# Kernel optimization log

Hardware: AMD Instinct MI355X
Metric: run time of the kernel (lower is better)

The kernel has to match this reference:

```python
import jax, jax.numpy as jnp
import numpy as np

KSIZE = 7
NSPIX = 196


def _unfold(x, k):
    # x: (T, C, H, W) -> (T, C, k*k, H, W), reflect padding, torch Unfold ordering
    p = (k - 1) // 2
    T, C, H, W = x.shape
    xp = jnp.pad(x, ((0, 0), (0, 0), (p, p), (p, p)), mode='reflect')
    return jnp.stack([xp[:, :, i:i + H, j:j + W] for i in range(k) for j in range(k)], axis=2)


def setup_inputs() -> dict:
    key = jax.random.key(0)
    k1, k2, k3, k4, k5 = jax.random.split(key, 5)
    T, C, H, W = 2, 64, 160, 160
    fan_in = C * KSIZE * KSIZE
    x = jax.random.normal(k1, (T, C, H, W), jnp.float32)
    spix = jax.random.randint(k2, (T, H, W), 0, NSPIX, jnp.int32)
    W_lin = jax.random.normal(k3, (C, fan_in), jnp.float32) / np.sqrt(fan_in)
    b_lin = jax.random.normal(k4, (C,), jnp.float32) * 0.01
    w_scale = jax.random.normal(k5, (C,), jnp.float32) / np.sqrt(C)
    b_scale = jnp.zeros((1,), jnp.float32)
    return {"x": x, "spix": spix, "W_lin": W_lin, "b_lin": b_lin,
            "w_scale": w_scale, "b_scale": b_scale}


def reference(x, spix, W_lin, b_lin, w_scale, b_scale):
    T, C, H, W = x.shape
    K2 = KSIZE * KSIZE
    O = W_lin.shape[0]
    p = (KSIZE - 1) // 2

    # unfold(x) with reflect padding -> patches (T, C, K2, H, W)
    patches = _unfold(x, KSIZE)

    # unfold(spix) -> neighbor superpixel ids per pixel (T, K2, H, W)
    sp = jnp.pad(spix, ((0, 0), (p, p), (p, p)), mode='reflect')
    nb = jnp.stack([sp[:, i:i + H, j:j + W] for i in range(KSIZE) for j in range(KSIZE)], axis=1)

    # per-frame superpixel mean pooling (bist.get_pooled_video): down (T, S, C)
    seg = (spix.astype(jnp.int32) + jnp.arange(T, dtype=jnp.int32)[:, None, None] * NSPIX).reshape(-1)
    feats = x.transpose(0, 2, 3, 1).reshape(-1, C)  # (T*H*W, C)
    sums = jax.ops.segment_sum(feats, seg, num_segments=T * NSPIX).reshape(T, NSPIX, C)
    cnts = jax.ops.segment_sum(jnp.ones((seg.shape[0],), x.dtype), seg,
                               num_segments=T * NSPIX).reshape(T, NSPIX, 1)
    down = sums / jnp.maximum(cnts, 1.0)

    # squared pairwise distances between superpixel means: pwd (T, S, S)
    sq = jnp.sum(down * down, axis=-1)
    pwd = jnp.maximum(sq[:, :, None] + sq[:, None, :]
                      - 2.0 * jnp.einsum('tsc,tuc->tsu', down, down), 0.0)

    # sims[t,k,h,w] = ||mean(spix[t,h,w]) - mean(nb[t,k,h,w])||^2
    tidx = jnp.arange(T)[:, None, None, None]
    sims = pwd[tidx, spix[:, None, :, :], nb]  # (T, K2, H, W)

    # scale = 10 * softplus(1x1-conv(x / ||x||_c))  -> (T, H, W)
    xn = x / (jnp.linalg.norm(x, axis=1, keepdims=True) + 1e-10)
    scale = 10.0 * jax.nn.softplus(jnp.einsum('c,tchw->thw', w_scale, xn) + b_scale[0])

    # apply_norm 'exp_max' over the kernel-tap axis
    rw = jnp.exp(-scale[:, None, :, :] * sims)  # (T, K2, H, W)
    rw = rw / (1e-5 + jnp.max(rw, axis=1, keepdims=True))

    # dynamic conv: out[t,o,h,w] = sum_{c,k} W[o,c,k] * patches[t,c,k,h,w] * rw[t,k,h,w] + b[o]
    out = jnp.einsum('ock,tckhw,tkhw->tohw', W_lin.reshape(O, C, K2), patches, rw)
    return out + b_lin[None, :, None, None]
```

## Files before the change

### kernel.cpp

```cpp
#include <hip/hip_runtime.h>
#include <math.h>

#define TT 2
#define CC 64
#define HH 160
#define WW 160
#define KS 7
#define K2 49
#define NSPIX 196
#define HWSZ (HH*WW)
#define PAD 3
#define OO 64
#define FANIN (CC*K2)
#define TS 8
#define PS (TS+KS-1)
#define NPOS (PS*PS)
#define XROW 72

#define NCHUNK 50
#define CHUNKPIX 512
#define NCG 8

typedef short short8 __attribute__((ext_vector_type(8)));
typedef float f32x16 __attribute__((ext_vector_type(16)));

__device__ __forceinline__ int reflect(int i, int n) {
    if (i < 0) i = -i;
    if (i >= n) i = 2*n - 2 - i;
    return i;
}

__device__ __forceinline__ unsigned short f2bf(float f) {
    unsigned int u = __float_as_uint(f);
    unsigned int r = (u + 0x7FFFu + ((u >> 16) & 1u)) >> 16;
    return (unsigned short)r;
}
__device__ __forceinline__ float bf2f(unsigned short s) {
    return __uint_as_float(((unsigned int)s) << 16);
}

__global__ void k_wb(const float* __restrict__ Wl, unsigned short* __restrict__ Wb) {
    int idx = blockIdx.x*256 + threadIdx.x;
    if (idx >= 2*K2*4*64*8) return;
    int j   = idx & 7;
    int ln  = (idx >> 3) & 63;
    int kc  = (idx >> 9) & 3;
    int tap = (idx >> 11) % K2;
    int qo  = idx / (K2 << 11);
    int o = qo*32 + (ln & 31);
    int c = kc*16 + (ln >> 5)*8 + j;
    Wb[idx] = f2bf(Wl[o*FANIN + c*K2 + tap]);
}

__global__ __launch_bounds__(256) void k_seg(const float* __restrict__ x,
                                             const int* __restrict__ spix,
                                             float* __restrict__ partials,
                                             float* __restrict__ cntp) {
    __shared__ float ls[8*200];
    __shared__ float lcnt[200];
    int tid = threadIdx.x;
    int cg = blockIdx.x & 7;
    int rest = blockIdx.x >> 3;
    int ch = rest % NCHUNK;
    int t  = rest / NCHUNK;

    for (int i = tid; i < 8*200; i += 256) ls[i] = 0.f;
    if (cg == 0) for (int i = tid; i < 200; i += 256) lcnt[i] = 0.f;
    __syncthreads();

    int base = ch*CHUNKPIX;
    const float* xb = x + ((size_t)t*CC + cg*8)*HWSZ;
    #pragma unroll
    for (int i = 0; i < CHUNKPIX; i += 256) {
        int pix = base + i + tid;
        int s = spix[t*HWSZ + pix];
        if (cg == 0) atomicAdd(&lcnt[s], 1.0f);
        #pragma unroll
        for (int j = 0; j < 8; ++j) atomicAdd(&ls[j*200 + s], xb[(size_t)j*HWSZ + pix]);
    }
    __syncthreads();

    float* pb = partials + ((size_t)(t*NCHUNK + ch)*NSPIX)*CC + cg*8;
    for (int i = tid; i < 8*NSPIX; i += 256) {
        int s = i >> 3, j = i & 7;
        pb[s*CC + j] = ls[j*200 + s];
    }
    if (cg == 0)
        for (int i = tid; i < NSPIX; i += 256)
            cntp[(t*NCHUNK + ch)*NSPIX + i] = lcnt[i];
}

__global__ __launch_bounds__(256) void k_red(const float* __restrict__ partials,
                                             const float* __restrict__ cntp,
                                             float* __restrict__ down,
                                             float* __restrict__ sq) {
    int ts = blockIdx.x*4 + threadIdx.y;
    if (ts >= TT*NSPIX) return;
    int t = ts / NSPIX, s = ts - t*NSPIX;
    int c = threadIdx.x;

    const float* pb = partials + ((size_t)t*NCHUNK*NSPIX + s)*CC + c;
    float acc = 0.f;
    #pragma unroll 10
    for (int ch = 0; ch < NCHUNK; ++ch) acc += pb[(size_t)ch*NSPIX*CC];

    float cv = (c < NCHUNK) ? cntp[(t*NCHUNK + c)*NSPIX + s] : 0.f;
    #pragma unroll
    for (int off = 1; off < 64; off <<= 1) cv += __shfl_xor(cv, off, 64);

    float d = acc / fmaxf(cv, 1.0f);
    down[ts*CC + c] = d;
    float v = d*d;
    #pragma unroll
    for (int off = 1; off < 64; off <<= 1) v += __shfl_xor(v, off, 64);
    if (c == 0) sq[ts] = v;
}

__global__ void k_pwd(const float* __restrict__ down, const float* __restrict__ sq,
                      float* __restrict__ pwd) {
    int tid = blockIdx.x*256 + threadIdx.x;
    if (tid >= TT*NSPIX*NSPIX) return;
    int t = tid / (NSPIX*NSPIX); int r = tid - t*NSPIX*NSPIX;
    int s = r / NSPIX, u = r - (r / NSPIX)*NSPIX;
    const float* ds = down + (t*NSPIX + s)*CC;
    const float* du = down + (t*NSPIX + u)*CC;
    float dot = 0.f;
    #pragma unroll 4
    for (int c = 0; c < CC; ++c) dot += ds[c]*du[c];
    float v = sq[t*NSPIX + s] + sq[t*NSPIX + u] - 2.f*dot;
    pwd[tid] = fmaxf(v, 0.f);
}

__global__ void k_scale(const float* __restrict__ x, const float* __restrict__ wsc,
                        const float* __restrict__ bsc, float* __restrict__ scale) {
    int pix = blockIdx.x*256 + threadIdx.x;
    if (pix >= TT*HWSZ) return;
    int t = pix / HWSZ, hw = pix - t*HWSZ;
    const float* xs = x + (size_t)t*CC*HWSZ + hw;
    float s1 = 0.f, s2 = 0.f;
    #pragma unroll 8
    for (int c = 0; c < CC; ++c) { float v = xs[c*HWSZ]; s1 += wsc[c]*v; s2 += v*v; }
    float z = s1/(sqrtf(s2) + 1e-10f) + bsc[0];
    float sp_ = (z > 0.f) ? z + log1pf(expf(-z)) : log1pf(expf(z));
    scale[pix] = 10.f*sp_;
}

__global__ __launch_bounds__(256, 4) void k_main(
    const float* __restrict__ x, const int* __restrict__ spix,
    const unsigned short* __restrict__ Wb, const float* __restrict__ b_lin,
    const float* __restrict__ pwd, const float* __restrict__ scale,
    float* __restrict__ out)
{
    __shared__ unsigned short xpT[NPOS*XROW];
    __shared__ unsigned short rwb[K2*64];
    __shared__ int   sp[NPOS];
    __shared__ float mxp[4*64];
    __shared__ float mxl[64];

    int bid = blockIdx.x;
    int t = bid / 400;
    int r = bid - t*400;
    int th0 = (r / 20)*TS, tw0 = (r - (r/20)*20)*TS;
    int tid = threadIdx.y*64 + threadIdx.x;

    for (int i = tid; i < NPOS; i += 256) {
        int rr = reflect(th0 + i/PS - PAD, HH);
        int cc = reflect(tw0 + i%PS - PAD, WW);
        sp[i] = spix[t*HWSZ + rr*WW + cc];
    }
    for (int i = tid; i < NPOS*32; i += 256) {
        int pos = i % NPOS;
        int cp  = i / NPOS;
        int rr = reflect(th0 + pos/PS - PAD, HH);
        int cc = reflect(tw0 + pos%PS - PAD, WW);
        const float* xs = x + ((size_t)t*CC + 2*cp)*HWSZ + rr*WW + cc;
        float v0 = xs[0];
        float v1 = xs[HWSZ];
        unsigned int pk = (unsigned int)f2bf(v0) | ((unsigned int)f2bf(v1) << 16);
        *(unsigned int*)&xpT[pos*XROW + cp*2] = pk;
    }
    __syncthreads();

    int p_ = threadIdx.x;
    int ty = threadIdx.y;
    int py0 = p_ >> 3, px0 = p_ & 7;
    {
        float sc = scale[t*HWSZ + (th0 + py0)*WW + (tw0 + px0)];
        int s0 = sp[(py0 + PAD)*PS + (px0 + PAD)];
        const float* pr = pwd + (t*NSPIX + s0)*NSPIX;
        float pmax = 0.f;
        for (int k = ty; k < K2; k += 4) {
            int di = k/KS, dj = k - di*KS;
            int nb = sp[(py0 + di)*PS + (px0 + dj)];
            float v = expf(-sc * pr[nb]);
            rwb[k*64 + p_] = f2bf(v);
            pmax = fmaxf(pmax, v);
        }
        mxp[ty*64 + p_] = pmax;
    }
    __syncthreads();
    if (ty == 0) {
        float m = fmaxf(fmaxf(mxp[p_], mxp[64 + p_]), fmaxf(mxp[128 + p_], mxp[192 + p_]));
        mxl[p_] = 1.f/(1e-5f + m);
    }
    __syncthreads();
    {
        float s = mxl[p_];
        for (int k = ty; k < K2; k += 4)
            rwb[k*64 + p_] = f2bf(bf2f(rwb[k*64 + p_]) * s);
    }
    __syncthreads();

    int ln = threadIdx.x;
    int wv = __builtin_amdgcn_readfirstlane(threadIdx.y);
    int qo = wv >> 1, qp = wv & 1;
    int p  = qp*32 + (ln & 31);
    int ppy = p >> 3, ppx = p & 7;
    int k8 = (ln >> 5)*8;

    const unsigned short* Wq = Wb + (size_t)qo*K2*4*512 + ln*8;

    f32x16 acc;
    #pragma unroll
    for (int i = 0; i < 16; ++i) acc[i] = 0.f;

    int di = 0, dj = 0;
    for (int tap = 0; tap < K2; ++tap) {
        const unsigned short* wt = Wq + tap*2048;
        short8 A0 = *(const short8*)(wt);
        short8 A1 = *(const short8*)(wt + 512);
        short8 A2 = *(const short8*)(wt + 1024);
        short8 A3 = *(const short8*)(wt + 1536);

        int pos = (ppy + di)*PS + (ppx + dj);
        const unsigned short* bb = &xpT[pos*XROW + k8];
        short8 B0 = *(const short8*)(bb);
        short8 B1 = *(const short8*)(bb + 16);
        short8 B2 = *(const short8*)(bb + 32);
        short8 B3 = *(const short8*)(bb + 48);

        f32x16 C;
        #pragma unroll
        for (int i = 0; i < 16; ++i) C[i] = 0.f;
        C = __builtin_amdgcn_mfma_f32_32x32x16_bf16(A0, B0, C, 0, 0, 0);
        C = __builtin_amdgcn_mfma_f32_32x32x16_bf16(A1, B1, C, 0, 0, 0);
        C = __builtin_amdgcn_mfma_f32_32x32x16_bf16(A2, B2, C, 0, 0, 0);
        C = __builtin_amdgcn_mfma_f32_32x32x16_bf16(A3, B3, C, 0, 0, 0);

        float rwv = bf2f(rwb[tap*64 + p]);
        #pragma unroll
        for (int i = 0; i < 16; ++i) acc[i] = fmaf(C[i], rwv, acc[i]);

        if (++dj == KS) { dj = 0; ++di; }
    }

    int h = th0 + ppy, w = tw0 + ppx;
    int row_hi = 4*(ln >> 5);
    float* ob = out + (size_t)t*OO*HWSZ + h*WW + w;
    #pragma unroll
    for (int rg = 0; rg < 16; ++rg) {
        int o = qo*32 + (rg & 3) + 8*(rg >> 2) + row_hi;
        ob[(size_t)o*HWSZ] = acc[rg] + b_lin[o];
    }
}

extern "C" void kernel_launch(void* const* d_in, const int* in_sizes, int n_in,
                              void* d_out, int out_size, void* d_ws, size_t ws_size,
                              hipStream_t stream) {
    const float* x    = (const float*)d_in[0];
    const int*   spix = (const int*)d_in[1];
    const float* Wl   = (const float*)d_in[2];
    const float* bl   = (const float*)d_in[3];
    const float* wsc  = (const float*)d_in[4];
    const float* bsc  = (const float*)d_in[5];
    float* out = (float*)d_out;

    float* ws    = (float*)d_ws;
    float* down  = ws;
    float* sq    = down + TT*NSPIX*CC;
    float* pwd   = sq   + TT*NSPIX;
    float* scale = pwd  + TT*NSPIX*NSPIX;
    float* cntp  = scale + TT*HWSZ;
    float* parts = cntp + TT*NCHUNK*NSPIX;
    unsigned short* Wb = (unsigned short*)(parts + (size_t)TT*NCHUNK*NSPIX*CC);

    k_wb  <<<(2*K2*4*64*8 + 255)/256, 256, 0, stream>>>(Wl, Wb);
    k_seg <<<TT*NCHUNK*NCG, 256, 0, stream>>>(x, spix, parts, cntp);
    {
        dim3 blk(64, 4, 1);
        k_red <<<(TT*NSPIX + 3)/4, blk, 0, stream>>>(parts, cntp, down, sq);
    }
    k_pwd <<<(TT*NSPIX*NSPIX + 255)/256, 256, 0, stream>>>(down, sq, pwd);
    k_scale<<<(TT*HWSZ + 255)/256, 256, 0, stream>>>(x, wsc, bsc, scale);

    dim3 blk(64, 4, 1);
    k_main<<<TT*(HH/TS)*(WW/TS), blk, 0, stream>>>(x, spix, Wb, bl, pwd, scale, out);
}
```

Before: 166.7 us.

## Fuse prep kernels, swizzle LDS patch layout, split MFMA work by channel half

Merges the weight-conversion, segment-sum and scale kernels into one launch that branches on block index, which cuts the number of launches. In the main kernel, the padded LDS row layout is replaced by an XOR-swizzled 64-wide layout so each B fragment read stays free of bank conflicts without wasted padding. Each wave now covers all 64 outputs over half of the input channels, so every B load feeds two MFMA chains. The two halves are then summed through shared memory before the store. This costs an extra accumulator (more registers) and an extra reduction step with syncs.

```diff
diff --git a/kernel.cpp b/kernel.cpp
--- a/kernel.cpp
+++ b/kernel.cpp
@@ -15,7 +15,6 @@
 #define TS 8
 #define PS (TS+KS-1)
 #define NPOS (PS*PS)
-#define XROW 72
 
 #define NCHUNK 50
 #define CHUNKPIX 512
@@ -39,55 +38,78 @@
     return __uint_as_float(((unsigned int)s) << 16);
 }
 
-__global__ void k_wb(const float* __restrict__ Wl, unsigned short* __restrict__ Wb) {
-    int idx = blockIdx.x*256 + threadIdx.x;
-    if (idx >= 2*K2*4*64*8) return;
-    int j   = idx & 7;
-    int ln  = (idx >> 3) & 63;
-    int kc  = (idx >> 9) & 3;
-    int tap = (idx >> 11) % K2;
-    int qo  = idx / (K2 << 11);
-    int o = qo*32 + (ln & 31);
-    int c = kc*16 + (ln >> 5)*8 + j;
-    Wb[idx] = f2bf(Wl[o*FANIN + c*K2 + tap]);
-}
-
-__global__ __launch_bounds__(256) void k_seg(const float* __restrict__ x,
-                                             const int* __restrict__ spix,
-                                             float* __restrict__ partials,
-                                             float* __restrict__ cntp) {
+__global__ __launch_bounds__(256) void k_prep(const float* __restrict__ x,
+                                              const int* __restrict__ spix,
+                                              const float* __restrict__ Wl,
+                                              const float* __restrict__ wsc,
+                                              const float* __restrict__ bsc,
+                                              float* __restrict__ partials,
+                                              float* __restrict__ cntp,
+                                              float* __restrict__ scale,
+                                              unsigned short* __restrict__ Wb) {
     __shared__ float ls[8*200];
     __shared__ float lcnt[200];
+    int bid = blockIdx.x;
     int tid = threadIdx.x;
-    int cg = blockIdx.x & 7;
-    int rest = blockIdx.x >> 3;
-    int ch = rest % NCHUNK;
-    int t  = rest / NCHUNK;
-
-    for (int i = tid; i < 8*200; i += 256) ls[i] = 0.f;
-    if (cg == 0) for (int i = tid; i < 200; i += 256) lcnt[i] = 0.f;
-    __syncthreads();
-
-    int base = ch*CHUNKPIX;
-    const float* xb = x + ((size_t)t*CC + cg*8)*HWSZ;
-    #pragma unroll
-    for (int i = 0; i < CHUNKPIX; i += 256) {
-        int pix = base + i + tid;
-        int s = spix[t*HWSZ + pix];
-        if (cg == 0) atomicAdd(&lcnt[s], 1.0f);
-        #pragma unroll
-        for (int j = 0; j < 8; ++j) atomicAdd(&ls[j*200 + s], xb[(size_t)j*HWSZ + pix]);
-    }
-    __syncthreads();
-
-    float* pb = partials + ((size_t)(t*NCHUNK + ch)*NSPIX)*CC + cg*8;
-    for (int i = tid; i < 8*NSPIX; i += 256) {
-        int s = i >> 3, j = i & 7;
-        pb[s*CC + j] = ls[j*200 + s];
-    }
-    if (cg == 0)
-        for (int i = tid; i < NSPIX; i += 256)
-            cntp[(t*NCHUNK + ch)*NSPIX + i] = lcnt[i];
+
+    if (bid < 800) {
+        int cg = bid & 7;
+        int rest = bid >> 3;
+        int ch = rest % NCHUNK;
+        int t  = rest / NCHUNK;
+
+        for (int i = tid; i < 8*200; i += 256) ls[i] = 0.f;
+        if (cg == 0) for (int i = tid; i < 200; i += 256) lcnt[i] = 0.f;
+        __syncthreads();
+
+        int base = ch*CHUNKPIX;
+        const float* xb = x + ((size_t)t*CC + cg*8)*HWSZ;
+        #pragma unroll
+        for (int i = 0; i < CHUNKPIX; i += 256) {
+            int pix = base + i + tid;
+            int s = spix[t*HWSZ + pix];
+            if (cg == 0) atomicAdd(&lcnt[s], 1.0f);
+            #pragma unroll
+            for (int j = 0; j < 8; ++j) atomicAdd(&ls[j*200 + s], xb[(size_t)j*HWSZ + pix]);
+        }
+        __syncthreads();
+
+        float* pb = partials + ((size_t)(t*NCHUNK + ch)*NSPIX)*CC + cg*8;
+        for (int i = tid; i < 8*NSPIX; i += 256) {
+            int s = i >> 3, j = i & 7;
+            pb[s*CC + j] = ls[j*200 + s];
+        }
+        if (cg == 0)
+            for (int i = tid; i < NSPIX; i += 256)
+                cntp[(t*NCHUNK + ch)*NSPIX + i] = lcnt[i];
+    } else if (bid < 1000) {
+        int pix = (bid - 800)*256 + tid;
+        if (pix < TT*HWSZ) {
+            int t = pix / HWSZ, hw = pix - t*HWSZ;
+            const float* xs = x + (size_t)t*CC*HWSZ + hw;
+            float s1 = 0.f, s2 = 0.f;
+            #pragma unroll 8
+            for (int c = 0; c < CC; ++c) { float v = xs[c*HWSZ]; s1 += wsc[c]*v; s2 += v*v; }
+            float z = s1/(sqrtf(s2) + 1e-10f) + bsc[0];
+            float sp_ = (z > 0.f) ? z + log1pf(expf(-z)) : log1pf(expf(z));
+            scale[pix] = 10.f*sp_;
+        }
+    } else {
+        int row = (bid - 1000)*256 + tid;
+        if (row < 2*K2*4*64) {
+            int ln  = row & 63;
+            int kc  = (row >> 6) & 3;
+            int tq  = row >> 8;
+            int tap = tq % K2;
+            int qo  = tq / K2;
+            int o = qo*32 + (ln & 31);
+            int cb = kc*16 + (ln >> 5)*8;
+            unsigned short* dst = Wb + (size_t)row*8;
+            const float* src = Wl + (size_t)o*FANIN + tap;
+            #pragma unroll
+            for (int j = 0; j < 8; ++j) dst[j] = f2bf(src[(size_t)(cb + j)*K2]);
+        }
+    }
 }
 
 __global__ __launch_bounds__(256) void k_red(const float* __restrict__ partials,
@@ -131,27 +153,13 @@
     pwd[tid] = fmaxf(v, 0.f);
 }
 
-__global__ void k_scale(const float* __restrict__ x, const float* __restrict__ wsc,
-                        const float* __restrict__ bsc, float* __restrict__ scale) {
-    int pix = blockIdx.x*256 + threadIdx.x;
-    if (pix >= TT*HWSZ) return;
-    int t = pix / HWSZ, hw = pix - t*HWSZ;
-    const float* xs = x + (size_t)t*CC*HWSZ + hw;
-    float s1 = 0.f, s2 = 0.f;
-    #pragma unroll 8
-    for (int c = 0; c < CC; ++c) { float v = xs[c*HWSZ]; s1 += wsc[c]*v; s2 += v*v; }
-    float z = s1/(sqrtf(s2) + 1e-10f) + bsc[0];
-    float sp_ = (z > 0.f) ? z + log1pf(expf(-z)) : log1pf(expf(z));
-    scale[pix] = 10.f*sp_;
-}
-
 __global__ __launch_bounds__(256, 4) void k_main(
     const float* __restrict__ x, const int* __restrict__ spix,
     const unsigned short* __restrict__ Wb, const float* __restrict__ b_lin,
     const float* __restrict__ pwd, const float* __restrict__ scale,
     float* __restrict__ out)
 {
-    __shared__ unsigned short xpT[NPOS*XROW];
+    __shared__ unsigned short xpT[NPOS*64];
     __shared__ unsigned short rwb[K2*64];
     __shared__ int   sp[NPOS];
     __shared__ float mxp[4*64];
@@ -177,7 +185,8 @@
         float v0 = xs[0];
         float v1 = xs[HWSZ];
         unsigned int pk = (unsigned int)f2bf(v0) | ((unsigned int)f2bf(v1) << 16);
-        *(unsigned int*)&xpT[pos*XROW + cp*2] = pk;
+        int idx = pos*64 + (((cp >> 2) ^ (pos & 7)) << 3) + (cp & 3)*2;
+        *(unsigned int*)&xpT[idx] = pk;
     }
     __syncthreads();
 
@@ -213,54 +222,75 @@
 
     int ln = threadIdx.x;
     int wv = __builtin_amdgcn_readfirstlane(threadIdx.y);
-    int qo = wv >> 1, qp = wv & 1;
+    int qp = wv & 1, kh = wv >> 1;
     int p  = qp*32 + (ln & 31);
     int ppy = p >> 3, ppx = p & 7;
-    int k8 = (ln >> 5)*8;
-
-    const unsigned short* Wq = Wb + (size_t)qo*K2*4*512 + ln*8;
-
-    f32x16 acc;
+    int kc0 = 2*kh, kc1 = 2*kh + 1;
+    int lhi = ln >> 5;
+
+    const unsigned short* A00b = Wb + (size_t)kc0*512 + ln*8;
+    const unsigned short* A10b = A00b + (size_t)K2*4*512;
+
+    f32x16 Czero;
     #pragma unroll
-    for (int i = 0; i < 16; ++i) acc[i] = 0.f;
+    for (int i = 0; i < 16; ++i) Czero[i] = 0.f;
+    f32x16 acc0 = Czero, acc1 = Czero;
+
+    int jc0 = 2*kc0 + lhi, jc1 = 2*kc1 + lhi;
 
     int di = 0, dj = 0;
+    #pragma unroll 7
     for (int tap = 0; tap < K2; ++tap) {
-        const unsigned short* wt = Wq + tap*2048;
-        short8 A0 = *(const short8*)(wt);
-        short8 A1 = *(const short8*)(wt + 512);
-        short8 A2 = *(const short8*)(wt + 1024);
-        short8 A3 = *(const short8*)(wt + 1536);
+        const unsigned short* a0 = A00b + tap*2048;
+        short8 A00 = *(const short8*)(a0);
+        short8 A01 = *(const short8*)(a0 + 512);
+        const unsigned short* a1 = A10b + tap*2048;
+        short8 A10 = *(const short8*)(a1);
+        short8 A11 = *(const short8*)(a1 + 512);
 
         int pos = (ppy + di)*PS + (ppx + dj);
-        const unsigned short* bb = &xpT[pos*XROW + k8];
-        short8 B0 = *(const short8*)(bb);
-        short8 B1 = *(const short8*)(bb + 16);
-        short8 B2 = *(const short8*)(bb + 32);
-        short8 B3 = *(const short8*)(bb + 48);
-
-        f32x16 C;
-        #pragma unroll
-        for (int i = 0; i < 16; ++i) C[i] = 0.f;
-        C = __builtin_amdgcn_mfma_f32_32x32x16_bf16(A0, B0, C, 0, 0, 0);
-        C = __builtin_amdgcn_mfma_f32_32x32x16_bf16(A1, B1, C, 0, 0, 0);
-        C = __builtin_amdgcn_mfma_f32_32x32x16_bf16(A2, B2, C, 0, 0, 0);
-        C = __builtin_amdgcn_mfma_f32_32x32x16_bf16(A3, B3, C, 0, 0, 0);
+        int sw  = pos & 7;
+        const unsigned short* bbase = &xpT[pos*64];
+        short8 B0 = *(const short8*)(bbase + ((jc0 ^ sw) << 3));
+        short8 B1 = *(const short8*)(bbase + ((jc1 ^ sw) << 3));
+
+        f32x16 C0 = __builtin_amdgcn_mfma_f32_32x32x16_bf16(A00, B0, Czero, 0, 0, 0);
+        C0 = __builtin_amdgcn_mfma_f32_32x32x16_bf16(A01, B1, C0, 0, 0, 0);
+        f32x16 C1 = __builtin_amdgcn_mfma_f32_32x32x16_bf16(A10, B0, Czero, 0, 0, 0);
+        C1 = __builtin_amdgcn_mfma_f32_32x32x16_bf16(A11, B1, C1, 0, 0, 0);
 
         float rwv = bf2f(rwb[tap*64 + p]);
         #pragma unroll
-        for (int i = 0; i < 16; ++i) acc[i] = fmaf(C[i], rwv, acc[i]);
+        for (int i = 0; i < 16; ++i) acc0[i] = fmaf(C0[i], rwv, acc0[i]);
+        #pragma unroll
+        for (int i = 0; i < 16; ++i) acc1[i] = fmaf(C1[i], rwv, acc1[i]);
 
         if (++dj == KS) { dj = 0; ++di; }
     }
 
-    int h = th0 + ppy, w = tw0 + ppx;
-    int row_hi = 4*(ln >> 5);
-    float* ob = out + (size_t)t*OO*HWSZ + h*WW + w;
-    #pragma unroll
-    for (int rg = 0; rg < 16; ++rg) {
-        int o = qo*32 + (rg & 3) + 8*(rg >> 2) + row_hi;
-        ob[(size_t)o*HWSZ] = acc[rg] + b_lin[o];
+    __syncthreads();
+    float* red = (float*)xpT;
+    if (kh == 1) {
+        #pragma unroll
+        for (int i = 0; i < 16; ++i) {
+            red[i*128 + qp*64 + ln]        = acc0[i];
+            red[(16 + i)*128 + qp*64 + ln] = acc1[i];
+        }
+    }
+    __syncthreads();
+    if (kh == 0) {
+        int h = th0 + ppy, w = tw0 + ppx;
+        int row_hi = 4*lhi;
+        float* ob = out + (size_t)t*OO*HWSZ + h*WW + w;
+        #pragma unroll
+        for (int rg = 0; rg < 16; ++rg) {
+            float v0 = acc0[rg] + red[rg*128 + qp*64 + ln];
+            float v1 = acc1[rg] + red[(16 + rg)*128 + qp*64 + ln];
+            int o0 = (rg & 3) + 8*(rg >> 2) + row_hi;
+            int o1 = 32 + o0;
+            ob[(size_t)o0*HWSZ] = v0 + b_lin[o0];
+            ob[(size_t)o1*HWSZ] = v1 + b_lin[o1];
+        }
     }
 }
 
@@ -284,14 +314,12 @@
     float* parts = cntp + TT*NCHUNK*NSPIX;
     unsigned short* Wb = (unsigned short*)(parts + (size_t)TT*NCHUNK*NSPIX*CC);
 
-    k_wb  <<<(2*K2*4*64*8 + 255)/256, 256, 0, stream>>>(Wl, Wb);
-    k_seg <<<TT*NCHUNK*NCG, 256, 0, stream>>>(x, spix, parts, cntp);
+    k_prep<<<1196, 256, 0, stream>>>(x, spix, Wl, wsc, bsc, parts, cntp, scale, Wb);
     {
         dim3 blk(64, 4, 1);
         k_red <<<(TT*NSPIX + 3)/4, blk, 0, stream>>>(parts, cntp, down, sq);
     }
     k_pwd <<<(TT*NSPIX*NSPIX + 255)/256, 256, 0, stream>>>(down, sq, pwd);
-    k_scale<<<(TT*HWSZ + 255)/256, 256, 0, stream>>>(x, wsc, bsc, scale);
 
     dim3 blk(64, 4, 1);
     k_main<<<TT*(HH/TS)*(WW/TS), blk, 0, stream>>>(x, spix, Wb, bl, pwd, scale, out);
```

Measured after the change: 162.5 us. -2.5%, faster.
